# Performance work log

Measured on AMD Instinct MI355X. Metric: run time of the kernel, lower is better.

## Reference

```python
import jax, jax.numpy as jnp
import numpy as np

SIX = 6

def _make_table():
    # p_q_2_lut_table: [2*SIX, 2**SIX] binary selection matrix.
    # Flattened p_q order: indices 0..5 are (1-x)_j, indices 6..11 are x_j.
    t = np.zeros((2 * SIX, 2 ** SIX), dtype=np.float32)
    for i in range(2 ** SIX):
        bins = format(i, '06b')
        for j in range(SIX):
            if bins[j] == '0':
                t[j + SIX, i] = 1.0
            else:
                t[j, i] = 1.0
    return t

_P_Q_2_LUT_TABLE = jnp.asarray(_make_table())  # [12, 64]


def setup_inputs() -> dict:
    key = jax.random.key(0)
    k1, k2 = jax.random.split(key)
    B, N = 1024, 2048
    inputs = jax.random.uniform(k1, (B, N, SIX), dtype=jnp.float32)  # probabilities
    lut = jax.random.normal(k2, (N, 2 ** SIX), dtype=jnp.float32)
    return {"inputs": inputs, "lut": lut}


def reference(inputs, lut):
    eps = 1e-07
    # p_q: [B, N, 12] = concat(1 - x, x) along last axis (matches [2,6] flatten)
    p_q = jnp.concatenate([1.0 - inputs, inputs], axis=-1)
    p_q = jax.nn.relu(p_q) + eps
    p_q_log = jnp.log(p_q)
    # log-matmul-exp against binary selection table -> per-entry LUT probabilities
    lut_p = jnp.exp(jnp.einsum('bnk,kt->bnt', p_q_log, _P_Q_2_LUT_TABLE))  # [B,N,64]
    # weight by sigmoid(lut) [N,64] broadcast over batch, reduce over table axis
    output = jnp.sum(lut_p * jax.nn.sigmoid(lut)[None, :, :], axis=-1)  # [B,N]
    return output
```

## Files before the change

kernel.cpp:

```cpp
#include <hip/hip_runtime.h>

#define EPS 1e-7f

__global__ __launch_bounds__(256, 4) void lut_kernel(const float* __restrict__ in,
                                                     const float* __restrict__ lut,
                                                     float* __restrict__ out,
                                                     int N) {
    __shared__ float wsm[64][65];

    const int t  = threadIdx.x;
    const int n0 = blockIdx.x * 64;
    const int n  = n0 + (t & 63);
    const int b0 = blockIdx.y * 32 + (t >> 6);

    {
        const float4* lp = reinterpret_cast<const float4*>(lut + (size_t)n0 * 64);
        const int r  = t >> 2;
        const int c4 = t & 3;
        #pragma unroll
        for (int p = 0; p < 4; ++p) {
            const int s = c4 + p * 4;
            float4 v = lp[r * 16 + s];
            wsm[r][s * 4 + 0] = 1.0f / (1.0f + __expf(-v.x));
            wsm[r][s * 4 + 1] = 1.0f / (1.0f + __expf(-v.y));
            wsm[r][s * 4 + 2] = 1.0f / (1.0f + __expf(-v.z));
            wsm[r][s * 4 + 3] = 1.0f / (1.0f + __expf(-v.w));
        }
    }
    __syncthreads();

    float w[64];
    {
        const int nl = t & 63;
        #pragma unroll
        for (int k = 0; k < 16; ++k) {
            float4 v = *reinterpret_cast<const float4*>(&wsm[nl][k * 4]);
            w[4*k+0] = v.x; w[4*k+1] = v.y; w[4*k+2] = v.z; w[4*k+3] = v.w;
        }
    }

    const size_t base = (size_t)b0 * N + n;
    const float2* ip = reinterpret_cast<const float2*>(in + base * 6);
    float* op = out + base;
    const size_t bstride2 = (size_t)4 * N * 3;

    float2 p0 = ip[0], p1 = ip[1], p2 = ip[2];

    #pragma unroll 2
    for (int it = 0; it < 8; ++it) {
        const float2 v0 = p0, v1 = p1, v2 = p2;
        if (it < 7) {
            const float2* np = ip + (size_t)(it + 1) * bstride2;
            p0 = np[0]; p1 = np[1]; p2 = np[2];
        }
        const float x0 = v0.x, x1 = v0.y, x2 = v1.x,
                    x3 = v1.y, x4 = v2.x, x5 = v2.y;

        const float A0 = fmaxf(x0, 0.0f) + EPS, B0 = fmaxf(1.0f - x0, 0.0f) + EPS;
        const float A1 = fmaxf(x1, 0.0f) + EPS, B1 = fmaxf(1.0f - x1, 0.0f) + EPS;
        const float A2 = fmaxf(x2, 0.0f) + EPS, B2 = fmaxf(1.0f - x2, 0.0f) + EPS;
        const float A3 = fmaxf(x3, 0.0f) + EPS, B3 = fmaxf(1.0f - x3, 0.0f) + EPS;
        const float A4 = fmaxf(x4, 0.0f) + EPS, B4 = fmaxf(1.0f - x4, 0.0f) + EPS;
        const float A5 = fmaxf(x5, 0.0f) + EPS, B5 = fmaxf(1.0f - x5, 0.0f) + EPS;

        float t01[4];
        t01[0] = A0 * A1;  t01[1] = A0 * B1;
        t01[2] = B0 * A1;  t01[3] = B0 * B1;
        float t34[4];
        t34[0] = A3 * A4;  t34[1] = A3 * B4;
        t34[2] = B3 * A4;  t34[3] = B3 * B4;

        float tlo[8];
        #pragma unroll
        for (int h = 0; h < 8; ++h)
            tlo[h] = t34[h >> 1] * ((h & 1) ? B5 : A5);

        float acc = 0.0f;
        #pragma unroll
        for (int h = 0; h < 8; ++h) {
            float s = 0.0f;
            #pragma unroll
            for (int l = 0; l < 8; ++l) s = fmaf(tlo[l], w[h * 8 + l], s);
            const float thi = t01[h >> 1] * ((h & 1) ? B2 : A2);
            acc = fmaf(thi, s, acc);
        }
        op[(size_t)it * 4 * N] = acc;
    }
}

extern "C" void kernel_launch(void* const* d_in, const int* in_sizes, int n_in,
                              void* d_out, int out_size, void* d_ws, size_t ws_size,
                              hipStream_t stream) {
    const float* inputs = (const float*)d_in[0];
    const float* lut    = (const float*)d_in[1];
    float* out = (float*)d_out;

    const int lut_sz = in_sizes[1];
    const int N = lut_sz / 64;
    const int B = in_sizes[0] / (6 * N);

    dim3 grid(N / 64, B / 32);
    lut_kernel<<<grid, 256, 0, stream>>>(inputs, lut, out, N);
}
```

Measured before the change: 17.22 us.

## Stage input tiles through double-buffered shared memory with coalesced float4 loads

Input rows are now loaded with fully coalesced float4 reads of whole 8-batch x 64-column tiles into a double-buffered LDS staging area. Each thread then reads its six values from shared memory instead of issuing strided float2 global loads. The next tile is prefetched into registers while the current one is consumed. In exchange the kernel uses more shared memory (24 KB) and adds a block barrier per stage, which may reduce occupancy.

New measurement: 17.41 us. About the same (+1.1%).

```diff
diff --git a/kernel.cpp b/kernel.cpp
--- a/kernel.cpp
+++ b/kernel.cpp
@@ -6,85 +6,99 @@
                                                      const float* __restrict__ lut,
                                                      float* __restrict__ out,
                                                      int N) {
-    __shared__ float wsm[64][65];
+    __shared__ __align__(16) float smem[6144];
 
     const int t  = threadIdx.x;
+    const int nl = t & 63;
+    const int w  = t >> 6;
     const int n0 = blockIdx.x * 64;
-    const int n  = n0 + (t & 63);
-    const int b0 = blockIdx.y * 32 + (t >> 6);
+    const int n  = n0 + nl;
+    const int b0base = blockIdx.y * 32;
 
+    const size_t rowF4 = (size_t)N * 6 / 4;
+    const float4* inF4 = reinterpret_cast<const float4*>(in);
+
+    const size_t off0 = (size_t)(t / 96) * rowF4 + (t % 96);
+    const size_t off1 = (size_t)((t + 256) / 96) * rowF4 + ((t + 256) % 96);
+    const size_t off2 = (size_t)((t + 512) / 96) * rowF4 + ((t + 512) % 96);
+    const size_t sbase = (size_t)b0base * rowF4 + (size_t)n0 * 6 / 4;
+
+    float4 r0 = inF4[sbase + off0];
+    float4 r1 = inF4[sbase + off1];
+    float4 r2 = inF4[sbase + off2];
+
+    float wreg[64];
     {
+        float (*wsm)[65] = reinterpret_cast<float(*)[65]>(smem);
         const float4* lp = reinterpret_cast<const float4*>(lut + (size_t)n0 * 64);
-        const int r  = t >> 2;
-        const int c4 = t & 3;
+        const int rr = t >> 2, c4 = t & 3;
         #pragma unroll
         for (int p = 0; p < 4; ++p) {
-            const int s = c4 + p * 4;
-            float4 v = lp[r * 16 + s];
-            wsm[r][s * 4 + 0] = 1.0f / (1.0f + __expf(-v.x));
-            wsm[r][s * 4 + 1] = 1.0f / (1.0f + __expf(-v.y));
-            wsm[r][s * 4 + 2] = 1.0f / (1.0f + __expf(-v.z));
-            wsm[r][s * 4 + 3] = 1.0f / (1.0f + __expf(-v.w));
+            const int sidx = c4 + p * 4;
+            float4 v = lp[rr * 16 + sidx];
+            wsm[rr][sidx * 4 + 0] = 1.0f / (1.0f + __expf(-v.x));
+            wsm[rr][sidx * 4 + 1] = 1.0f / (1.0f + __expf(-v.y));
+            wsm[rr][sidx * 4 + 2] = 1.0f / (1.0f + __expf(-v.z));
+            wsm[rr][sidx * 4 + 3] = 1.0f / (1.0f + __expf(-v.w));
         }
-    }
-    __syncthreads();
-
-    float w[64];
-    {
-        const int nl = t & 63;
+        __syncthreads();
         #pragma unroll
-        for (int k = 0; k < 16; ++k) {
-            float4 v = *reinterpret_cast<const float4*>(&wsm[nl][k * 4]);
-            w[4*k+0] = v.x; w[4*k+1] = v.y; w[4*k+2] = v.z; w[4*k+3] = v.w;
-        }
+        for (int k = 0; k < 64; ++k)
+            wreg[k] = wsm[nl][k];
+        __syncthreads();
     }
 
-    const size_t base = (size_t)b0 * N + n;
-    const float2* ip = reinterpret_cast<const float2*>(in + base * 6);
-    float* op = out + base;
-    const size_t bstride2 = (size_t)4 * N * 3;
+    float* op = out + (size_t)(b0base + w) * N + n;
 
-    float2 p0 = ip[0], p1 = ip[1], p2 = ip[2];
+    #pragma unroll
+    for (int s = 0; s < 4; ++s) {
+        float* bcur = smem + (s & 1) * 3072;
+        float4* bv = reinterpret_cast<float4*>(bcur);
+        bv[t] = r0; bv[t + 256] = r1; bv[t + 512] = r2;
+        if (s < 3) {
+            const size_t nb = sbase + (size_t)(8 * (s + 1)) * rowF4;
+            r0 = inF4[nb + off0]; r1 = inF4[nb + off1]; r2 = inF4[nb + off2];
+        }
+        __syncthreads();
 
-    #pragma unroll 2
-    for (int it = 0; it < 8; ++it) {
-        const float2 v0 = p0, v1 = p1, v2 = p2;
-        if (it < 7) {
-            const float2* np = ip + (size_t)(it + 1) * bstride2;
-            p0 = np[0]; p1 = np[1]; p2 = np[2];
+        #pragma unroll
+        for (int h = 0; h < 2; ++h) {
+            const int it = 2 * s + h;
+            const int row = w + h * 4;
+            const float* src = bcur + row * 384 + nl * 6;
+            const float x0 = src[0], x1 = src[1], x2 = src[2],
+                        x3 = src[3], x4 = src[4], x5 = src[5];
+
+            const float A0 = fmaxf(x0, 0.0f) + EPS, B0 = fmaxf(1.0f - x0, 0.0f) + EPS;
+            const float A1 = fmaxf(x1, 0.0f) + EPS, B1 = fmaxf(1.0f - x1, 0.0f) + EPS;
+            const float A2 = fmaxf(x2, 0.0f) + EPS, B2 = fmaxf(1.0f - x2, 0.0f) + EPS;
+            const float A3 = fmaxf(x3, 0.0f) + EPS, B3 = fmaxf(1.0f - x3, 0.0f) + EPS;
+            const float A4 = fmaxf(x4, 0.0f) + EPS, B4 = fmaxf(1.0f - x4, 0.0f) + EPS;
+            const float A5 = fmaxf(x5, 0.0f) + EPS, B5 = fmaxf(1.0f - x5, 0.0f) + EPS;
+
+            float t01[4];
+            t01[0] = A0 * A1;  t01[1] = A0 * B1;
+            t01[2] = B0 * A1;  t01[3] = B0 * B1;
+            float t34[4];
+            t34[0] = A3 * A4;  t34[1] = A3 * B4;
+            t34[2] = B3 * A4;  t34[3] = B3 * B4;
+
+            float tlo[8];
+            #pragma unroll
+            for (int hh = 0; hh < 8; ++hh)
+                tlo[hh] = t34[hh >> 1] * ((hh & 1) ? B5 : A5);
+
+            float acc = 0.0f;
+            #pragma unroll
+            for (int hh = 0; hh < 8; ++hh) {
+                float sum = 0.0f;
+                #pragma unroll
+                for (int l = 0; l < 8; ++l) sum = fmaf(tlo[l], wreg[hh * 8 + l], sum);
+                const float thi = t01[hh >> 1] * ((hh & 1) ? B2 : A2);
+                acc = fmaf(thi, sum, acc);
+            }
+            op[(size_t)it * 4 * N] = acc;
         }
-        const float x0 = v0.x, x1 = v0.y, x2 = v1.x,
-                    x3 = v1.y, x4 = v2.x, x5 = v2.y;
-
-        const float A0 = fmaxf(x0, 0.0f) + EPS, B0 = fmaxf(1.0f - x0, 0.0f) + EPS;
-        const float A1 = fmaxf(x1, 0.0f) + EPS, B1 = fmaxf(1.0f - x1, 0.0f) + EPS;
-        const float A2 = fmaxf(x2, 0.0f) + EPS, B2 = fmaxf(1.0f - x2, 0.0f) + EPS;
-        const float A3 = fmaxf(x3, 0.0f) + EPS, B3 = fmaxf(1.0f - x3, 0.0f) + EPS;
-        const float A4 = fmaxf(x4, 0.0f) + EPS, B4 = fmaxf(1.0f - x4, 0.0f) + EPS;
-        const float A5 = fmaxf(x5, 0.0f) + EPS, B5 = fmaxf(1.0f - x5, 0.0f) + EPS;
-
-        float t01[4];
-        t01[0] = A0 * A1;  t01[1] = A0 * B1;
-        t01[2] = B0 * A1;  t01[3] = B0 * B1;
-        float t34[4];
-        t34[0] = A3 * A4;  t34[1] = A3 * B4;
-        t34[2] = B3 * A4;  t34[3] = B3 * B4;
-
-        float tlo[8];
-        #pragma unroll
-        for (int h = 0; h < 8; ++h)
-            tlo[h] = t34[h >> 1] * ((h & 1) ? B5 : A5);
-
-        float acc = 0.0f;
-        #pragma unroll
-        for (int h = 0; h < 8; ++h) {
-            float s = 0.0f;
-            #pragma unroll
-            for (int l = 0; l < 8; ++l) s = fmaf(tlo[l], w[h * 8 + l], s);
-            const float thi = t01[h >> 1] * ((h & 1) ? B2 : A2);
-            acc = fmaf(thi, s, acc);
-        }
-        op[(size_t)it * 4 * N] = acc;
     }
 }
 
```
